# Kernel tuning notes

Measured on AMD Instinct MI355X. Metric: run time of the kernel, lower is better.

The kernel has to match this reference:

```python
import jax, jax.numpy as jnp
import numpy as np

B, T, C, H = 2, 2048, 1024, 16
D = C // H  # head dim = 64

def setup_inputs() -> dict:
    key = jax.random.key(0)
    k1, k2 = jax.random.split(key)
    x = jax.random.normal(k1, (B, T, C), dtype=jnp.float32)
    W_attn = jax.random.normal(k2, (3 * C, C), dtype=jnp.float32) * 0.02
    return {"x": x, "W_attn": W_attn}

def reference(x, W_attn):
    Bx, Tx, Cx = x.shape
    qkv = jnp.einsum('btc,fc->btf', x, W_attn)  # fused QKV projection (bias=False)
    q, k, v = jnp.split(qkv, 3, axis=-1)
    # [B, H, T, D]
    q = q.reshape(Bx, Tx, H, D).transpose(0, 2, 1, 3)
    k = k.reshape(Bx, Tx, H, D).transpose(0, 2, 1, 3)
    v = v.reshape(Bx, Tx, H, D).transpose(0, 2, 1, 3)
    scale = 1.0 / jnp.sqrt(jnp.asarray(D, dtype=q.dtype))
    scores = jnp.einsum('bhqd,bhkd->bhqk', q, k) * scale  # [B,H,T,T]
    causal = jnp.tril(jnp.ones((Tx, Tx), dtype=bool))
    scores = jnp.where(causal[None, None], scores, jnp.asarray(-jnp.inf, dtype=scores.dtype))
    attn = jax.nn.softmax(scores, axis=-1)
    y = jnp.einsum('bhqk,bhkd->bhqd', attn, v)
    y = y.transpose(0, 2, 1, 3).reshape(Bx, Tx, Cx)  # merge heads; dropout=0 at eval
    return y
```

## Files before the change

kernel.cpp:

```cpp
#include <hip/hip_runtime.h>
#include <hip/hip_bf16.h>

#define Bn 2
#define Tn 2048
#define Cn 1024
#define Hn 16
#define Dn 64
#define Mdim 4096
#define Ndim 3072
#define Kdim 1024

typedef unsigned short u16;
typedef __attribute__((ext_vector_type(8))) short bf16x8;
typedef __attribute__((ext_vector_type(4))) float f32x4;

__device__ __forceinline__ u16 f2bf(float v) {
    unsigned int x = __builtin_bit_cast(unsigned int, v);
    unsigned int r = (x + 0x7fffu + ((x >> 16) & 1u)) >> 16;
    return (u16)r;
}

__device__ __forceinline__ unsigned int pack2(float a, float b) {
    return (unsigned int)f2bf(a) | ((unsigned int)f2bf(b) << 16);
}

__device__ __forceinline__ unsigned int cvt_pk_bf16(float lo, float hi) {
    unsigned int r;
    asm("v_cvt_pk_bf16_f32 %0, %1, %2" : "=v"(r) : "v"(lo), "v"(hi));
    return r;
}

__device__ __forceinline__ void async16(const void* g, void* l) {
    __builtin_amdgcn_global_load_lds(
        (const __attribute__((address_space(1))) void*)g,
        (__attribute__((address_space(3))) void*)(unsigned int)(unsigned long long)l,
        16, 0, 0);
}

__device__ __forceinline__ int probe_inline(const unsigned int* __restrict__ X, int tid) {
    const int lane = tid & 63;
    int cnt = 0;
    #pragma unroll
    for (int i = 0; i < 8; i++) {
        unsigned int e = (X[lane * 8 + i] >> 7) & 0xFFu;
        cnt += (e >= 100u && e < 134u) ? 1 : 0;
    }
    #pragma unroll
    for (int off = 1; off < 64; off <<= 1) cnt += __shfl_xor(cnt, off);
    return cnt > 256 ? 1 : 0;
}

#define NXC ((size_t)Mdim * Kdim / 8)
#define NWC ((size_t)Ndim * Kdim / 8)

__global__ __launch_bounds__(256) void convert_in(
        const void* __restrict__ Xv, const void* __restrict__ Wv,
        u16* __restrict__ Xb, u16* __restrict__ Wb, int* __restrict__ flag) {
    const int isbf = probe_inline((const unsigned int*)Xv, threadIdx.x);
    if (blockIdx.x == 0 && threadIdx.x == 0) *flag = isbf;
    size_t i = (size_t)blockIdx.x * 256 + threadIdx.x;
    if (i >= NXC + NWC) return;
    const void* src; u16* dst; size_t off;
    if (i < NXC) { src = Xv; dst = Xb; off = i; }
    else         { src = Wv; dst = Wb; off = i - NXC; }
    if (isbf) {
        ((uint4*)dst)[off] = ((const uint4*)src)[off];
    } else {
        const float4* s = (const float4*)src + off * 2;
        float4 a = s[0], b = s[1];
        ((uint4*)dst)[off] = (uint4){pack2(a.x, a.y), pack2(a.z, a.w),
                                     pack2(b.x, b.y), pack2(b.z, b.w)};
    }
}

#define NTq (Kdim / 64)

#define PBAR() do { asm volatile("" ::: "memory"); \
                    __builtin_amdgcn_s_barrier();  \
                    asm volatile("" ::: "memory"); } while (0)
#define VMW(n) asm volatile("s_waitcnt vmcnt(" #n ")" ::: "memory")

#define QSTAGE_A(QIDX, BUF, KOFF) \
    async16(Xb + (size_t)(m0 + (QIDX) * 64 + srow) * Kdim + (KOFF) + gc, \
            &sA[BUF][(QIDX) * 4096 + w * 512])
#define QSTAGE_B(QIDX, BUF, KOFF) \
    async16(Wb + (size_t)(n0 + (QIDX) * 64 + srow) * Kdim + (KOFF) + gc, \
            &sB[BUF][(QIDX) * 4096 + w * 512])

#define RDA(MQ, BUF) do {                                                  \
    _Pragma("unroll")                                                      \
    for (int mt = 0; mt < 4; mt++) {                                       \
        const u16* p = &sA[BUF][(wm + (MQ) * 64 + mt * 16 + r16) * 64];    \
        af[mt][0] = *(const bf16x8*)(p + cx0);                             \
        af[mt][1] = *(const bf16x8*)(p + (cx0 ^ 32));                      \
    } } while (0)

#define RDB(NQ, BUF) do {                                                  \
    _Pragma("unroll")                                                      \
    for (int nt = 0; nt < 2; nt++) {                                       \
        const u16* p = &sB[BUF][(wn + (NQ) * 32 + nt * 16 + r16) * 64];    \
        bf[NQ][nt][0] = *(const bf16x8*)(p + cx0);                         \
        bf[NQ][nt][1] = *(const bf16x8*)(p + (cx0 ^ 32));                  \
    } } while (0)

#define MM(MQ, NQ) do {                                                    \
    __builtin_amdgcn_s_setprio(1);                                         \
    _Pragma("unroll")                                                      \
    for (int mt = 0; mt < 4; mt++)                                         \
        _Pragma("unroll")                                                  \
        for (int nt = 0; nt < 2; nt++) {                                   \
            acc[(MQ)*4+mt][(NQ)*2+nt] = __builtin_amdgcn_mfma_f32_16x16x32_bf16( \
                af[mt][0], bf[NQ][nt][0], acc[(MQ)*4+mt][(NQ)*2+nt], 0,0,0);     \
            acc[(MQ)*4+mt][(NQ)*2+nt] = __builtin_amdgcn_mfma_f32_16x16x32_bf16( \
                af[mt][1], bf[NQ][nt][1], acc[(MQ)*4+mt][(NQ)*2+nt], 0,0,0);     \
        }                                                                  \
    __builtin_amdgcn_s_setprio(0);                                         \
} while (0)

__global__ __launch_bounds__(512, 2) void qkv_gemm(
        const u16* __restrict__ Xb, const u16* __restrict__ Wb,
        u16* __restrict__ Q, u16* __restrict__ Kc, u16* __restrict__ Vt) {
    __shared__ __align__(16) u16 sA[2][256 * 64];
    __shared__ __align__(16) u16 sB[2][256 * 64];

    const int tid  = threadIdx.x;
    const int lane = tid & 63;
    const int w    = tid >> 6;
    const int quad = lane >> 4;
    const int r16  = lane & 15;
    const int wm   = (w >> 2) * 128;
    const int wn   = (w & 3) * 64;

    const int l0 = blockIdx.x;
    const int nl = (l0 & 7) * 24 + (l0 >> 3);
    const int m0 = (nl / 12) * 256;
    const int n0 = (nl % 12) * 256;

    const int lr   = lane >> 3;
    const int gc   = ((lane & 7) ^ lr) * 8;
    const int srow = w * 8 + lr;

    const int cx0 = (quad ^ (r16 & 7)) * 8;

    f32x4 acc[8][4];
    #pragma unroll
    for (int i = 0; i < 8; i++)
        #pragma unroll
        for (int j = 0; j < 4; j++)
            acc[i][j] = (f32x4){0.f, 0.f, 0.f, 0.f};

    bf16x8 af[4][2];
    bf16x8 bf[2][2][2];

    #pragma unroll
    for (int q = 0; q < 4; q++) { QSTAGE_A(q, 0, 0); QSTAGE_B(q, 0, 0); }
    VMW(0);
    PBAR();

    int koff = 0;
    for (int kt = 0; kt < NTq; kt++) {
        const int cur = kt & 1, nxt = cur ^ 1;
        const bool pf = (kt + 1 < NTq);
        const int kn = koff + 64;
        RDA(0, cur); RDB(0, cur);
        if (pf) { QSTAGE_B(0, nxt, kn); QSTAGE_B(1, nxt, kn); }
        PBAR(); MM(0, 0); PBAR();
        RDB(1, cur);
        if (pf) { QSTAGE_B(2, nxt, kn); QSTAGE_B(3, nxt, kn); }
        VMW(4); PBAR(); MM(0, 1); PBAR();
        RDA(1, cur);
        if (pf) { QSTAGE_A(0, nxt, kn); QSTAGE_A(2, nxt, kn); }
        PBAR(); MM(1, 1); PBAR();
        if (pf) { QSTAGE_A(1, nxt, kn); QSTAGE_A(3, nxt, kn); }
        VMW(2); PBAR(); MM(1, 0); PBAR();
        koff = kn;
    }

    const int sect = n0 >> 10;
    #pragma unroll
    for (int mq = 0; mq < 2; mq++)
    #pragma unroll
    for (int mt = 0; mt < 4; mt++)
    #pragma unroll
    for (int nq = 0; nq < 2; nq++)
    #pragma unroll
    for (int nt = 0; nt < 2; nt++) {
        f32x4 v4 = acc[mq * 4 + mt][nq * 2 + nt];
        const int mBase = m0 + wm + mq * 64 + mt * 16 + quad * 4;
        const int f = n0 + wn + nq * 32 + nt * 16 + r16;
        const int b = mBase >> 11;
        const int t0 = mBase & 2047;
        const int h = (f >> 6) & 15;
        const int d = f & 63;
        const int bh = b * Hn + h;
        if (sect == 0) {
            #pragma unroll
            for (int r = 0; r < 4; r++)
                Q[((size_t)(bh * Tn + t0 + r)) * Dn + d] = f2bf(v4[r] * 0.125f);
        } else if (sect == 1) {
            #pragma unroll
            for (int r = 0; r < 4; r++)
                Kc[((size_t)(bh * Tn + t0 + r)) * Dn + d] = f2bf(v4[r]);
        } else {
            ushort4 pk4 = {f2bf(v4[0]), f2bf(v4[1]), f2bf(v4[2]), f2bf(v4[3])};
            *(ushort4*)(Vt + ((size_t)(bh * Dn + d)) * Tn + t0) = pk4;
        }
    }
}


#define SWZ(R, C) ((R) * 64 + (((C) * 8) ^ (((R) & 7) << 3)))

#define ASTG(KB, BUF) do {                                                     \
    const int kbase_ = (KB) * 64;                                              \
    if (w < 2) {                                                               \
        _Pragma("unroll")                                                      \
        for (int i_ = 0; i_ < 4; i_++) {                                       \
            const int seg = w * 4 + i_;            \
            async16(Kc + qkBase + (size_t)(kbase_ + seg * 8 + rl) * Dn + gc8,  \
                    &sK[BUF][seg * 512]);                                      \
        }                                                                      \
    } else {                                                                   \
        _Pragma("unroll")                                                      \
        for (int i_ = 0; i_ < 4; i_++) {                                       \
            const int seg = (w - 2) * 4 + i_;    \
            async16(Vt + vBase + (size_t)(seg * 8 + rl) * Tn + kbase_ + gc8,   \
                    &sV[BUF][seg * 512]);                                      \
        }                                                                      \
    }                                                                          \
} while (0)

#define ACOMP(KB, BUF) do {                                                    \
    const int kbase_ = (KB) * 64;                                              \
    const bool diag_ = ((KB) == nkb - 1);                                      \
    bf16x8 kf[4][2], vf[4][2];                                                 \
    _Pragma("unroll")                                                          \
    for (int nt = 0; nt < 4; nt++) {                                           \
        kf[nt][0] = *(const bf16x8*)&sK[BUF][SWZ(nt * 16 + r16, quad)];        \
        kf[nt][1] = *(const bf16x8*)&sK[BUF][SWZ(nt * 16 + r16, 4 + quad)];    \
    }                                                                          \
    _Pragma("unroll")                                                          \
    for (int dt = 0; dt < 4; dt++) {                                           \
        vf[dt][0] = *(const bf16x8*)&sV[BUF][SWZ(dt * 16 + r16, quad)];        \
        vf[dt][1] = *(const bf16x8*)&sV[BUF][SWZ(dt * 16 + r16, 4 + quad)];    \
    }                                                                          \
    _Pragma("unroll")                                                          \
    for (int mt = 0; mt < 2; mt++) {                                           \
        f32x4 s[4];                                                            \
        __builtin_amdgcn_s_setprio(1);                                         \
        _Pragma("unroll")                                                      \
        for (int nt = 0; nt < 4; nt++) {                                       \
            f32x4 z = (f32x4){-8.f, -8.f, -8.f, -8.f};                         \
            z = __builtin_amdgcn_mfma_f32_16x16x32_bf16(kf[nt][0], aq[mt][0], z, 0, 0, 0); \
            z = __builtin_amdgcn_mfma_f32_16x16x32_bf16(kf[nt][1], aq[mt][1], z, 0, 0, 0); \
            s[nt] = z;                                                         \
        }                                                                      \
        __builtin_amdgcn_s_setprio(0);                                         \
        if (diag_) {                                                           \
            const int query = qw0 + mt * 16 + r16;                             \
            _Pragma("unroll")                                                  \
            for (int nt = 0; nt < 4; nt++)                                     \
                _Pragma("unroll")                                              \
                for (int r = 0; r < 4; r++) {                                  \
                    int key = kbase_ + nt * 16 + quad * 4 + r;                 \
                    if (key > query) s[nt][r] = -1e30f;                        \
                }                                                              \
        }                                                                      \
        unsigned int pk[4][2];                                                 \
        _Pragma("unroll")                                                      \
        for (int nt = 0; nt < 4; nt++) {                                       \
            float p0 = __expf(s[nt][0]);                                       \
            float p1 = __expf(s[nt][1]);                                       \
            float p2 = __expf(s[nt][2]);                                       \
            float p3 = __expf(s[nt][3]);                                       \
            lacc[mt] += (p0 + p1) + (p2 + p3);                                 \
            pk[nt][0] = cvt_pk_bf16(p0, p1);                                   \
            pk[nt][1] = cvt_pk_bf16(p2, p3);                                   \
        }                                                                      \
        _Pragma("unroll")                                                      \
        for (int kc = 0; kc < 2; kc++) {                                       \
            int4 bq;                                                           \
            _Pragma("unroll")                                                  \
            for (int h_ = 0; h_ < 2; h_++) {                                   \
                unsigned int a = pk[kc * 2 + 0][h_];                           \
                unsigned int b = pk[kc * 2 + 1][h_];                           \
                auto t = __builtin_amdgcn_permlane32_swap(a, b, false, false); \
                auto u = __builtin_amdgcn_permlane16_swap(t[0], t[1], false, false); \
                ((unsigned int*)&bq)[0 + h_] = u[0];                           \
                ((unsigned int*)&bq)[2 + h_] = u[1];                           \
            }                                                                  \
            bf16x8 bqv = __builtin_bit_cast(bf16x8, bq);                       \
            __builtin_amdgcn_s_setprio(1);                                     \
            _Pragma("unroll")                                                  \
            for (int dt = 0; dt < 4; dt++)                                     \
                o[mt][dt] = __builtin_amdgcn_mfma_f32_16x16x32_bf16(           \
                    vf[dt][kc], bqv, o[mt][dt], 0, 0, 0);                      \
            __builtin_amdgcn_s_setprio(0);                                     \
        }                                                                      \
    }                                                                          \
} while (0)

__global__ __launch_bounds__(256, 2) void attn(
        const u16* __restrict__ Q, const u16* __restrict__ Kc,
        const u16* __restrict__ Vt, void* __restrict__ Y,
        const int* __restrict__ flag) {
    __shared__ __align__(16) u16 sK[4][4096];
    __shared__ __align__(16) u16 sV[4][4096];

    const int isbf = *flag;
    const int tid  = threadIdx.x;
    const int lane = tid & 63;
    const int w    = tid >> 6;
    const int quad = lane >> 4;
    const int r16  = lane & 15;
    const int bid  = blockIdx.x;
    const int bh   = bid & (Bn * Hn - 1);
    const int half = bid >> 8;
    const int j    = (bid & 255) >> 5;
    const int qt   = half ? j : (15 - j);
    const int qw0  = qt * 128 + w * 32;
    const int nt   = 2 * qt + 2;
    const int nkb  = 2 * qt + 1 + (w >> 1);
    const size_t qkBase = (size_t)bh * Tn * Dn;
    const size_t vBase  = (size_t)bh * Dn * Tn;
    const int bb = bh >> 4, hh = bh & 15;

    const int rl  = lane >> 3;
    const int gc8 = (((lane & 7) ^ rl)) * 8;

    bf16x8 aq[2][2];
    #pragma unroll
    for (int mt = 0; mt < 2; mt++) {
        const u16* qp = Q + qkBase + (size_t)(qw0 + mt * 16 + r16) * Dn;
        aq[mt][0] = *(const bf16x8*)(qp + quad * 8);
        aq[mt][1] = *(const bf16x8*)(qp + 32 + quad * 8);
    }

    float lacc[2] = {0.f, 0.f};
    f32x4 o[2][4];
    #pragma unroll
    for (int mt = 0; mt < 2; mt++)
        #pragma unroll
        for (int dt = 0; dt < 4; dt++) o[mt][dt] = (f32x4){0.f, 0.f, 0.f, 0.f};

    ASTG(0, 0);
    ASTG(1, 1);
    VMW(4);
    PBAR();

    for (int i = 0; i < nt; i++) {
        if (i + 2 < nt)      { ASTG(i + 2, (i + 2) & 3); VMW(8); }
        else if (i + 1 < nt) { VMW(4); }
        else                 { VMW(0); }
        PBAR();
        if (i < nkb) ACOMP(i, i & 3);
    }

    #pragma unroll
    for (int mt = 0; mt < 2; mt++) {
        float den = lacc[mt];
        den += __shfl_xor(den, 16);
        den += __shfl_xor(den, 32);
        float rden = 1.f / fmaxf(den, 1e-30f);
        int t = qw0 + mt * 16 + r16;
        #pragma unroll
        for (int dt = 0; dt < 4; dt++) {
            float v0 = o[mt][dt][0] * rden;
            float v1 = o[mt][dt][1] * rden;
            float v2 = o[mt][dt][2] * rden;
            float v3 = o[mt][dt][3] * rden;
            int c = hh * Dn + dt * 16 + quad * 4;
            size_t idx = ((size_t)(bb * Tn + t)) * Cn + c;
            if (isbf) {
                ushort4 pk4 = {f2bf(v0), f2bf(v1), f2bf(v2), f2bf(v3)};
                *(ushort4*)((u16*)Y + idx) = pk4;
            } else {
                float4 f4 = {v0, v1, v2, v3};
                *(float4*)((float*)Y + idx) = f4;
            }
        }
    }
}

extern "C" void kernel_launch(void* const* d_in, const int* in_sizes, int n_in,
                              void* d_out, int out_size, void* d_ws, size_t ws_size,
                              hipStream_t stream) {
    const void* X = d_in[0];
    const void* W = d_in[1];
    void* Y = d_out;

    const size_t per = (size_t)Bn * Hn * Tn * Dn;
    int* flag = (int*)d_ws;
    u16* Q  = (u16*)((char*)d_ws + 256);
    u16* Kc = Q + per;
    u16* Vt = Kc + per;
    u16* Xb = Vt + per;
    u16* Wb = Xb + (size_t)Mdim * Kdim;

    {
        const size_t nch = NXC + NWC;
        convert_in<<<dim3((unsigned)((nch + 255) / 256)), 256, 0, stream>>>(X, W, Xb, Wb, flag);
    }
    qkv_gemm<<<dim3((Mdim / 256) * (Ndim / 256)), 512, 0, stream>>>(Xb, Wb, Q, Kc, Vt);
    attn<<<dim3(Bn * Hn * (Tn / 128)), 256, 0, stream>>>(Q, Kc, Vt, Y, flag);
}
```

Before: 147.5 us.

## Retile QKV GEMM to 256x192 blocks and simplify K-loop pipeline

```diff
diff --git a/kernel.cpp b/kernel.cpp
--- a/kernel.cpp
+++ b/kernel.cpp
@@ -80,48 +80,46 @@
                     asm volatile("" ::: "memory"); } while (0)
 #define VMW(n) asm volatile("s_waitcnt vmcnt(" #n ")" ::: "memory")
 
-#define QSTAGE_A(QIDX, BUF, KOFF) \
+#define STGA(QIDX, BUF, KOFF) \
     async16(Xb + (size_t)(m0 + (QIDX) * 64 + srow) * Kdim + (KOFF) + gc, \
             &sA[BUF][(QIDX) * 4096 + w * 512])
-#define QSTAGE_B(QIDX, BUF, KOFF) \
+#define STGB(QIDX, BUF, KOFF) \
     async16(Wb + (size_t)(n0 + (QIDX) * 64 + srow) * Kdim + (KOFF) + gc, \
             &sB[BUF][(QIDX) * 4096 + w * 512])
 
-#define RDA(MQ, BUF) do {                                                  \
+#define RDAh(FR, MQ, BUF) do {                                             \
     _Pragma("unroll")                                                      \
     for (int mt = 0; mt < 4; mt++) {                                       \
         const u16* p = &sA[BUF][(wm + (MQ) * 64 + mt * 16 + r16) * 64];    \
-        af[mt][0] = *(const bf16x8*)(p + cx0);                             \
-        af[mt][1] = *(const bf16x8*)(p + (cx0 ^ 32));                      \
+        FR[mt][0] = *(const bf16x8*)(p + cx0);                             \
+        FR[mt][1] = *(const bf16x8*)(p + (cx0 ^ 32));                      \
     } } while (0)
 
-#define RDB(NQ, BUF) do {                                                  \
+#define RDBall(BUF) do {                                                   \
     _Pragma("unroll")                                                      \
-    for (int nt = 0; nt < 2; nt++) {                                       \
-        const u16* p = &sB[BUF][(wn + (NQ) * 32 + nt * 16 + r16) * 64];    \
-        bf[NQ][nt][0] = *(const bf16x8*)(p + cx0);                         \
-        bf[NQ][nt][1] = *(const bf16x8*)(p + (cx0 ^ 32));                  \
+    for (int nt = 0; nt < 3; nt++) {                                       \
+        const u16* p = &sB[BUF][(wn + nt * 16 + r16) * 64];                \
+        bfr[nt][0] = *(const bf16x8*)(p + cx0);                            \
+        bfr[nt][1] = *(const bf16x8*)(p + (cx0 ^ 32));                     \
     } } while (0)
 
-#define MM(MQ, NQ) do {                                                    \
-    __builtin_amdgcn_s_setprio(1);                                         \
+#define MMH(BASE, FR) do {                                                 \
     _Pragma("unroll")                                                      \
     for (int mt = 0; mt < 4; mt++)                                         \
         _Pragma("unroll")                                                  \
-        for (int nt = 0; nt < 2; nt++) {                                   \
-            acc[(MQ)*4+mt][(NQ)*2+nt] = __builtin_amdgcn_mfma_f32_16x16x32_bf16( \
-                af[mt][0], bf[NQ][nt][0], acc[(MQ)*4+mt][(NQ)*2+nt], 0,0,0);     \
-            acc[(MQ)*4+mt][(NQ)*2+nt] = __builtin_amdgcn_mfma_f32_16x16x32_bf16( \
-                af[mt][1], bf[NQ][nt][1], acc[(MQ)*4+mt][(NQ)*2+nt], 0,0,0);     \
+        for (int nt = 0; nt < 3; nt++) {                                   \
+            acc[(BASE)+mt][nt] = __builtin_amdgcn_mfma_f32_16x16x32_bf16(  \
+                FR[mt][0], bfr[nt][0], acc[(BASE)+mt][nt], 0, 0, 0);       \
+            acc[(BASE)+mt][nt] = __builtin_amdgcn_mfma_f32_16x16x32_bf16(  \
+                FR[mt][1], bfr[nt][1], acc[(BASE)+mt][nt], 0, 0, 0);       \
         }                                                                  \
-    __builtin_amdgcn_s_setprio(0);                                         \
 } while (0)
 
 __global__ __launch_bounds__(512, 2) void qkv_gemm(
         const u16* __restrict__ Xb, const u16* __restrict__ Wb,
         u16* __restrict__ Q, u16* __restrict__ Kc, u16* __restrict__ Vt) {
     __shared__ __align__(16) u16 sA[2][256 * 64];
-    __shared__ __align__(16) u16 sB[2][256 * 64];
+    __shared__ __align__(16) u16 sB[2][192 * 64];
 
     const int tid  = threadIdx.x;
     const int lane = tid & 63;
@@ -129,12 +127,12 @@
     const int quad = lane >> 4;
     const int r16  = lane & 15;
     const int wm   = (w >> 2) * 128;
-    const int wn   = (w & 3) * 64;
+    const int wn   = (w & 3) * 48;
 
     const int l0 = blockIdx.x;
-    const int nl = (l0 & 7) * 24 + (l0 >> 3);
-    const int m0 = (nl / 12) * 256;
-    const int n0 = (nl % 12) * 256;
+    const int nl = (l0 & 7) * 32 + (l0 >> 3);
+    const int m0 = (nl >> 4) * 256;
+    const int n0 = (nl & 15) * 192;
 
     const int lr   = lane >> 3;
     const int gc   = ((lane & 7) ^ lr) * 8;
@@ -142,52 +140,58 @@
 
     const int cx0 = (quad ^ (r16 & 7)) * 8;
 
-    f32x4 acc[8][4];
+    f32x4 acc[8][3];
     #pragma unroll
     for (int i = 0; i < 8; i++)
         #pragma unroll
-        for (int j = 0; j < 4; j++)
+        for (int j = 0; j < 3; j++)
             acc[i][j] = (f32x4){0.f, 0.f, 0.f, 0.f};
 
-    bf16x8 af[4][2];
-    bf16x8 bf[2][2][2];
-
-    #pragma unroll
-    for (int q = 0; q < 4; q++) { QSTAGE_A(q, 0, 0); QSTAGE_B(q, 0, 0); }
+    bf16x8 af[4][2], ag[4][2];
+    bf16x8 bfr[3][2];
+
+    #pragma unroll
+    for (int q = 0; q < 4; q++) STGA(q, 0, 0);
+    #pragma unroll
+    for (int q = 0; q < 3; q++) STGB(q, 0, 0);
     VMW(0);
     PBAR();
 
     int koff = 0;
     for (int kt = 0; kt < NTq; kt++) {
         const int cur = kt & 1, nxt = cur ^ 1;
-        const bool pf = (kt + 1 < NTq);
         const int kn = koff + 64;
-        RDA(0, cur); RDB(0, cur);
-        if (pf) { QSTAGE_B(0, nxt, kn); QSTAGE_B(1, nxt, kn); }
-        PBAR(); MM(0, 0); PBAR();
-        RDB(1, cur);
-        if (pf) { QSTAGE_B(2, nxt, kn); QSTAGE_B(3, nxt, kn); }
-        VMW(4); PBAR(); MM(0, 1); PBAR();
-        RDA(1, cur);
-        if (pf) { QSTAGE_A(0, nxt, kn); QSTAGE_A(2, nxt, kn); }
-        PBAR(); MM(1, 1); PBAR();
-        if (pf) { QSTAGE_A(1, nxt, kn); QSTAGE_A(3, nxt, kn); }
-        VMW(2); PBAR(); MM(1, 0); PBAR();
+        if (kt + 1 < NTq) {
+            #pragma unroll
+            for (int q = 0; q < 4; q++) STGA(q, nxt, kn);
+            #pragma unroll
+            for (int q = 0; q < 3; q++) STGB(q, nxt, kn);
+            VMW(7);
+        } else {
+            VMW(0);
+        }
+        PBAR();
+        RDAh(af, 0, cur);
+        RDBall(cur);
+        RDAh(ag, 1, cur);
+        __builtin_amdgcn_s_setprio(1);
+        MMH(0, af);
+        MMH(4, ag);
+        __builtin_amdgcn_s_setprio(0);
+        PBAR();
         koff = kn;
     }
 
-    const int sect = n0 >> 10;
-    #pragma unroll
-    for (int mq = 0; mq < 2; mq++)
+    #pragma unroll
+    for (int mh = 0; mh < 2; mh++)
     #pragma unroll
     for (int mt = 0; mt < 4; mt++)
     #pragma unroll
-    for (int nq = 0; nq < 2; nq++)
-    #pragma unroll
-    for (int nt = 0; nt < 2; nt++) {
-        f32x4 v4 = acc[mq * 4 + mt][nq * 2 + nt];
-        const int mBase = m0 + wm + mq * 64 + mt * 16 + quad * 4;
-        const int f = n0 + wn + nq * 32 + nt * 16 + r16;
+    for (int nt = 0; nt < 3; nt++) {
+        f32x4 v4 = acc[mh * 4 + mt][nt];
+        const int mBase = m0 + wm + mh * 64 + mt * 16 + quad * 4;
+        const int f = n0 + wn + nt * 16 + r16;
+        const int sect = f >> 10;
         const int b = mBase >> 11;
         const int t0 = mBase & 2047;
         const int h = (f >> 6) & 15;
@@ -401,6 +405,6 @@
         const size_t nch = NXC + NWC;
         convert_in<<<dim3((unsigned)((nch + 255) / 256)), 256, 0, stream>>>(X, W, Xb, Wb, flag);
     }
-    qkv_gemm<<<dim3((Mdim / 256) * (Ndim / 256)), 512, 0, stream>>>(Xb, Wb, Q, Kc, Vt);
+    qkv_gemm<<<dim3((Mdim / 256) * (Ndim / 192)), 512, 0, stream>>>(Xb, Wb, Q, Kc, Vt);
     attn<<<dim3(Bn * Hn * (Tn / 128)), 256, 0, stream>>>(Q, Kc, Vt, Y, flag);
 }
```

New measurement: 142.4 us. -3.5%, faster.
